# Kernel tuning notes

Measured on AMD Instinct MI355X. Metric: run time of the kernel, lower is better.

The kernel has to match this reference:

```python
import jax, jax.numpy as jnp
import numpy as np
import math

K, D_FEAT, L_FAC, N = 128, 1024, 16, 16384


def setup_inputs() -> dict:
    key = jax.random.key(0)
    k1, k2, k3, k4 = jax.random.split(key, 4)
    x = jax.random.normal(k1, (N, D_FEAT), dtype=jnp.float32)
    MU = 0.1 * jax.random.normal(k2, (K, D_FEAT), dtype=jnp.float32)
    A = 0.05 * jax.random.normal(k3, (K, D_FEAT, L_FAC), dtype=jnp.float32)
    # D must be positive (it is a per-feature noise std): uniform in [0.1, 0.5]
    D = jax.random.uniform(k4, (K, D_FEAT), dtype=jnp.float32, minval=0.1, maxval=0.5)
    PI = jnp.ones((K,), dtype=jnp.float32) / K
    return {"x": x, "PI": PI, "MU": MU, "A": A, "D": D}


def reference(x, PI, MU, A, D):
    # Faithful vectorized version of MFA._per_component_log_likelihood.
    k, d, l = A.shape
    iD = jnp.power(D, -2.0)                      # (K, d)  = 1/D^2
    iDA = iD[:, :, None] * A                     # (K, d, l)
    # Woodbury small matrix: L = I_l + A^T (iD * A)
    Lm = jnp.eye(l, dtype=A.dtype)[None] + jnp.einsum('kdl,kdm->klm', A, iDA)
    iL = jnp.linalg.inv(Lm)                      # (K, l, l)

    # y[k,n,:] = A^T (iD * (x_n - MU_k))  without materializing (K,N,d)
    y = jnp.einsum('nd,kdl->knl', x, iDA) - jnp.einsum('kd,kdl->kl', MU, iDA)[:, None, :]
    # term1[k,n] = sum_d iD[k,d] * (x_n - MU_k)^2, expanded to avoid (K,N,d)
    term1 = (jnp.einsum('nd,kd->kn', x * x, iD)
             - 2.0 * jnp.einsum('nd,kd->kn', x, iD * MU)
             + jnp.sum(iD * MU * MU, axis=1)[:, None])
    # quadratic correction: y^T iL y
    quad = jnp.einsum('knl,klm,knm->kn', y, iL, y)
    m_d = term1 - quad                           # (K, N) Mahalanobis distances

    det_L = jnp.linalg.slogdet(Lm)[1]            # (K,)
    log_det_Sigma = det_L - jnp.sum(jnp.log(iD), axis=1)
    log2pi = jnp.asarray(math.log(2.0 * math.pi), dtype=x.dtype)
    log_prob = -0.5 * ((d * log2pi + log_det_Sigma)[:, None] + m_d)  # (K, N)
    # NOTE: original adds raw PI (not log PI) -- replicated faithfully.
    return PI[None, :] + log_prob.T              # (N, K)
```

## Files before the change

### kernel.cpp

```cpp
#include <hip/hip_runtime.h>
#include <math.h>

typedef unsigned short ushort_t;
typedef unsigned char  uchar_t;
typedef __attribute__((ext_vector_type(8))) short short8v;
typedef __attribute__((ext_vector_type(4))) float f32x4;
typedef __attribute__((ext_vector_type(2))) long l64x2;

#define KCOMP 128
#define DF    1024
#define LF    16
#define NPTS  16384
#define LOG2PI 1.8378770664093453f

#define XQ_OFF    ((size_t)0)
#define XQ_BYTES  ((size_t)NPTS*DF)
#define BQ_OFF    (XQ_OFF + XQ_BYTES)
#define BQ_BYTES  ((size_t)2048*DF)
#define BSK_OFF   (BQ_OFF + BQ_BYTES)
#define BSK_BYTES ((size_t)KCOMP*2*DF*2)
#define CSK_OFF   (BSK_OFF + BSK_BYTES)
#define FULL_NEED (CSK_OFF + 512)

__device__ __forceinline__ ushort_t f2bf(float f) {
  union { float f; unsigned u; } v; v.f = f;
  unsigned u = v.u;
  return (ushort_t)((u + 0x7FFFu + ((u >> 16) & 1u)) >> 16);
}

#define GLOAD16(gp, lp) __builtin_amdgcn_global_load_lds( \
  (const __attribute__((address_space(1))) unsigned int*)(gp), \
  (__attribute__((address_space(3))) unsigned int*)(lp), 16, 0, 0)

#define DPPADD(x, ctrl) do { \
  int _yi = __builtin_amdgcn_update_dpp(0, __float_as_int(x), ctrl, 0xF, 0xF, true); \
  (x) += __int_as_float(_yi); } while (0)

__global__ __launch_bounds__(256) void mfa_pre(
    const float* __restrict__ PI, const float* __restrict__ MU,
    const float* __restrict__ A, const float* __restrict__ Dm,
    uchar_t* __restrict__ Bq, ushort_t* __restrict__ Bsk,
    float* __restrict__ csk)
{
  const int k = blockIdx.x, t = threadIdx.x;
  const int tl = t >> 4, tm = t & 15;
  __shared__ float As[64][16];
  __shared__ float iD64[64], MU64[64];
  __shared__ float R[16][17];
  __shared__ float rinv_s[16], zsh[16], bsh[16];
  __shared__ float red[64];
  __shared__ float sc_sumlog, sc_c3;

  float accL = 0.f, accb = 0.f, c3p = 0.f, slogp = 0.f;
  for (int ch = 0; ch < 16; ++ch) {
    __syncthreads();
    ((float4*)&As[0][0])[t] =
        ((const float4*)(A + (size_t)k*DF*LF + (size_t)ch*1024))[t];
    if (t < 64) {
      float dv = Dm[k*DF + ch*64 + t];
      iD64[t] = 1.f/(dv*dv);
      MU64[t] = MU[k*DF + ch*64 + t];
    }
    __syncthreads();
    #pragma unroll 4
    for (int dd = 0; dd < 64; ++dd)
      accL = fmaf(As[dd][tl]*iD64[dd], As[dd][tm], accL);
    if (tm == 0)
      for (int dd = 0; dd < 64; ++dd)
        accb = fmaf(iD64[dd]*MU64[dd], As[dd][tl], accb);
    if (t < 64) {
      c3p = fmaf(iD64[t]*MU64[t], MU64[t], c3p);
      slogp += logf(iD64[t]);
    }
  }
  __syncthreads();
  R[tl][tm] = accL + (tl == tm ? 1.f : 0.f);
  if (tm == 0) bsh[tl] = accb;
  if (t < 64) red[t] = slogp;
  __syncthreads();
  if (t == 0) { float s = 0.f; for (int i = 0; i < 64; ++i) s += red[i]; sc_sumlog = s; }
  __syncthreads();
  if (t < 64) red[t] = c3p;
  __syncthreads();
  if (t == 0) { float s = 0.f; for (int i = 0; i < 64; ++i) s += red[i]; sc_c3 = s; }

  for (int j = 0; j < 16; ++j) {
    __syncthreads();
    if (t == j) {
      float s = R[j][j];
      for (int i = 0; i < j; ++i) s -= R[j][i]*R[j][i];
      float rj = sqrtf(s);
      R[j][j] = rj; rinv_s[j] = 1.f/rj;
    }
    __syncthreads();
    if (t < 16 && t > j) {
      float s = R[t][j];
      for (int i = 0; i < j; ++i) s -= R[t][i]*R[j][i];
      R[t][j] = s * rinv_s[j];
    }
  }
  __syncthreads();
  if (t == 0) {
    float ldet = 0.f;
    for (int j = 0; j < 16; ++j) ldet += 2.f*logf(R[j][j]);
    float w[16], z[16];
    for (int j = 0; j < 16; ++j) {
      float s = bsh[j];
      for (int i = 0; i < j; ++i) s -= R[j][i]*w[i];
      w[j] = s*rinv_s[j];
    }
    for (int j = 15; j >= 0; --j) {
      float s = w[j];
      for (int i = j+1; i < 16; ++i) s -= R[i][j]*z[i];
      z[j] = s*rinv_s[j];
      zsh[j] = z[j];
    }
    float muh = sc_c3;
    for (int l = 0; l < 16; ++l) muh -= bsh[l]*zsh[l];
    csk[k] = PI[k] - 0.5f*((float)DF*LOG2PI + ldet - sc_sumlog) - 0.5f*muh;
  }
  __syncthreads();

  for (int it = 0; it < 4; ++it) {
    const int d = t + it*256;
    float dv = Dm[k*DF + d];
    float iD = 1.f/(dv*dv);
    float mu = MU[k*DF + d];
    float v[16], gg[16];
    #pragma unroll
    for (int l = 0; l < 16; ++l) v[l] = iD * A[((size_t)k*DF + d)*LF + l];
    #pragma unroll
    for (int j = 0; j < 16; ++j) {
      float s = v[j];
      #pragma unroll
      for (int i = 0; i < 16; ++i) if (i < j) s -= R[j][i]*gg[i];
      gg[j] = s * rinv_s[j];
    }
    float h = iD*mu;
    #pragma unroll
    for (int l = 0; l < 16; ++l) h -= v[l]*zsh[l];
    const int dd = d & 63;
    const size_t poff = (size_t)(d & ~63) + ((dd >> 3) & 3)*16 + (dd >> 5)*8 + (dd & 7);
    #pragma unroll
    for (int l = 0; l < 16; ++l) {
      int r8 = __builtin_amdgcn_cvt_pk_fp8_f32(gg[l], gg[l], 0, false);
      Bq[(size_t)(k*16 + l)*DF + poff] = (uchar_t)(r8 & 0xFF);
    }
    Bsk[(size_t)k*2*DF + d]      = f2bf(-2.f*h);
    Bsk[(size_t)k*2*DF + DF + d] = f2bf(iD);
  }
}

__global__ __launch_bounds__(256) void mfa_sk2q(
    const float* __restrict__ x, const ushort_t* __restrict__ Bsk,
    const float* __restrict__ csk, uchar_t* __restrict__ xq,
    float* __restrict__ out)
{
  __shared__ ushort_t xs[4096];
  __shared__ ushort_t x2s[4096];
  __shared__ ushort_t Bs[16384];
  const int t = threadIdx.x, lane = t & 63, wid = t >> 6;
  const int wc = wid;
  const int lr = lane & 15, lh = lane >> 4;
  const int n0 = blockIdx.x * 64;
  const int xr = t >> 2, xc = t & 3;

  f32x4 acc[4][2] = {};

  float4 v0, v1, v2, v3;
  {
    const float* xp = x + (size_t)(n0 + xr)*DF + xc*16;
    v0 = ((const float4*)xp)[0]; v1 = ((const float4*)xp)[1];
    v2 = ((const float4*)xp)[2]; v3 = ((const float4*)xp)[3];
  }

  for (int tt = 0; tt < 16; ++tt) {
    const int d0 = tt * 64;
    __syncthreads();
    {
      float e[16] = {v0.x,v0.y,v0.z,v0.w, v1.x,v1.y,v1.z,v1.w,
                     v2.x,v2.y,v2.z,v2.w, v3.x,v3.y,v3.z,v3.w};
      short8v b0, b1, q0, q1;
      #pragma unroll
      for (int i = 0; i < 8; ++i) {
        b0[i] = (short)f2bf(e[i]);     q0[i] = (short)f2bf(e[i]*e[i]);
        b1[i] = (short)f2bf(e[8+i]);   q1[i] = (short)f2bf(e[8+i]*e[8+i]);
      }
      const int ch0 = (xc*2) ^ (xr & 7), ch1 = (xc*2+1) ^ (xr & 7);
      *(short8v*)&xs[xr*64 + ch0*8]  = b0;
      *(short8v*)&xs[xr*64 + ch1*8]  = b1;
      *(short8v*)&x2s[xr*64 + ch0*8] = q0;
      *(short8v*)&x2s[xr*64 + ch1*8] = q1;
      int p0 = 0, p1 = 0, p2 = 0, p3 = 0;
      p0 = __builtin_amdgcn_cvt_pk_fp8_f32(e[0],  e[1],  p0, false);
      p0 = __builtin_amdgcn_cvt_pk_fp8_f32(e[2],  e[3],  p0, true);
      p1 = __builtin_amdgcn_cvt_pk_fp8_f32(e[4],  e[5],  p1, false);
      p1 = __builtin_amdgcn_cvt_pk_fp8_f32(e[6],  e[7],  p1, true);
      p2 = __builtin_amdgcn_cvt_pk_fp8_f32(e[8],  e[9],  p2, false);
      p2 = __builtin_amdgcn_cvt_pk_fp8_f32(e[10], e[11], p2, true);
      p3 = __builtin_amdgcn_cvt_pk_fp8_f32(e[12], e[13], p3, false);
      p3 = __builtin_amdgcn_cvt_pk_fp8_f32(e[14], e[15], p3, true);
      long lo = (long)(((unsigned long long)(unsigned)p1 << 32) | (unsigned)p0);
      long hi = (long)(((unsigned long long)(unsigned)p3 << 32) | (unsigned)p2);
      size_t base = (size_t)(n0 + xr)*DF + d0 + (xc & 1)*32 + (xc >> 1)*8;
      *(long*)&xq[base]      = lo;
      *(long*)&xq[base + 16] = hi;
    }
    #pragma unroll
    for (int j = 0; j < 8; ++j) {
      int v = (wid*8 + j)*8 + (lane >> 3);
      int g = (lane & 7) ^ (v & 7);
      const ushort_t* src = (v < 128)
        ? Bsk + (size_t)v*(2*DF) + d0 + g*8
        : Bsk + (size_t)(v - 128)*(2*DF) + DF + d0 + g*8;
      GLOAD16(src, (char*)Bs + (wid*8 + j)*1024);
    }
    __syncthreads();
    if (tt < 15) {
      const float* xp = x + (size_t)(n0 + xr)*DF + (d0 + 64) + xc*16;
      v0 = ((const float4*)xp)[0]; v1 = ((const float4*)xp)[1];
      v2 = ((const float4*)xp)[2]; v3 = ((const float4*)xp)[3];
    }
    __builtin_amdgcn_sched_barrier(0);
    #pragma unroll
    for (int ks = 0; ks < 2; ++ks) {
      const int cterm = ((ks*4 + lh) ^ (lr & 7)) * 8;
      short8v a_[4], a2_[4], bh[2], bi[2];
      #pragma unroll
      for (int rb = 0; rb < 4; ++rb) {
        a_[rb]  = *(const short8v*)&xs[(rb*16 + lr)*64 + cterm];
        a2_[rb] = *(const short8v*)&x2s[(rb*16 + lr)*64 + cterm];
      }
      #pragma unroll
      for (int cb = 0; cb < 2; ++cb) {
        int vh = wc*32 + cb*16 + lr;
        bh[cb] = *(const short8v*)&Bs[vh*64 + cterm];
        bi[cb] = *(const short8v*)&Bs[(128 + vh)*64 + cterm];
      }
      #pragma unroll
      for (int cb = 0; cb < 2; ++cb)
        #pragma unroll
        for (int rb = 0; rb < 4; ++rb) {
          acc[rb][cb] = __builtin_amdgcn_mfma_f32_16x16x32_bf16(a_[rb],  bh[cb], acc[rb][cb], 0,0,0);
          acc[rb][cb] = __builtin_amdgcn_mfma_f32_16x16x32_bf16(a2_[rb], bi[cb], acc[rb][cb], 0,0,0);
        }
    }
  }
  #pragma unroll
  for (int cb = 0; cb < 2; ++cb) {
    int comp = wc*32 + cb*16 + lr;
    float ck = csk[comp];
    #pragma unroll
    for (int rb = 0; rb < 4; ++rb)
      #pragma unroll
      for (int j = 0; j < 4; ++j) {
        int row = n0 + rb*16 + lh*4 + j;
        out[(size_t)row*KCOMP + comp] = ck - 0.5f*acc[rb][cb][j];
      }
  }
}

__global__ __launch_bounds__(512, 4) void mfa_gemm11(
    const uchar_t* __restrict__ xq, const uchar_t* __restrict__ Bq,
    float* __restrict__ out)
{
  __shared__ uchar_t smem[73728];
  const int t = threadIdx.x, lane = t & 63, wid = t >> 6;
  const int wm = wid & 1, wn = wid >> 1;
  const int lr = lane & 15, lh = lane >> 4;

  const int bid = blockIdx.x;
  const int xcd = bid & 7, ib = bid >> 3;
  const int rb = xcd*16 + (ib >> 3);
  const int cb = ib & 7;
  const int n0 = rb * 128, c0 = cb * 256;

  f32x4 acc[4][4] = {};

  const int js = (((lane & 3) ^ ((lane >> 3) & 3)) * 16);
  const uchar_t* srcP[3]; int dstO[3];
  #pragma unroll
  for (int q = 0; q < 3; ++q) {
    int id = wid*3 + q;
    if (id < 8) {
      int r = id*16 + (lane >> 2);
      srcP[q] = xq + (size_t)(n0 + r)*DF + js;
      dstO[q] = id*1024;
    } else {
      int cr = (id - 8)*16 + (lane >> 2);
      srcP[q] = Bq + (size_t)(c0 + cr)*DF + js;
      dstO[q] = 8192 + (id - 8)*1024;
    }
  }
  const int rsw = (lh ^ ((lr >> 1) & 3)) * 16;
  const int aO = (wm*64 + lr)*64 + rsw;
  const int bO = 8192 + (wn*64 + lr)*64 + rsw;

  #define STAGE11(slot, tt_) do { \
    _Pragma("unroll") \
    for (int q = 0; q < 3; ++q) \
      GLOAD16(srcP[q] + (tt_)*64, (char*)smem + (slot)*24576 + dstO[q] + ((lane)*16 & 1023)); \
  } while (0)

  STAGE11(0, 0);
  STAGE11(1, 1);

  for (int tt = 0; tt < 16; ++tt) {
    if (tt < 15) asm volatile("s_waitcnt vmcnt(3)" ::: "memory");
    else         asm volatile("s_waitcnt vmcnt(0)" ::: "memory");
    __builtin_amdgcn_s_barrier();
    if (tt + 2 <= 15) STAGE11((tt + 2) % 3, tt + 2);

    const char* lb = (const char*)smem + (tt % 3) * 24576;
    l64x2 a2[4], b2[4];
    #pragma unroll
    for (int rt = 0; rt < 4; ++rt) a2[rt] = *(const l64x2*)(lb + aO + rt*1024);
    #pragma unroll
    for (int ct = 0; ct < 4; ++ct) b2[ct] = *(const l64x2*)(lb + bO + ct*1024);

    __builtin_amdgcn_s_setprio(1);
    #pragma unroll
    for (int ct = 0; ct < 4; ++ct)
      #pragma unroll
      for (int rt = 0; rt < 4; ++rt)
        acc[rt][ct] = __builtin_amdgcn_mfma_f32_16x16x32_fp8_fp8(a2[rt][0], b2[ct][0], acc[rt][ct], 0,0,0);
    #pragma unroll
    for (int ct = 0; ct < 4; ++ct)
      #pragma unroll
      for (int rt = 0; rt < 4; ++rt)
        acc[rt][ct] = __builtin_amdgcn_mfma_f32_16x16x32_fp8_fp8(a2[rt][1], b2[ct][1], acc[rt][ct], 0,0,0);
    __builtin_amdgcn_s_setprio(0);
  }

  #pragma unroll
  for (int ct = 0; ct < 4; ++ct) {
    const int comp = cb*16 + wn*4 + ct;
    #pragma unroll
    for (int rt = 0; rt < 4; ++rt) {
      #pragma unroll
      for (int j = 0; j < 4; ++j) {
        float v = acc[rt][ct][j];
        float sq = v*v;
        DPPADD(sq, 0xB1);
        DPPADD(sq, 0x4E);
        DPPADD(sq, 0x124);
        DPPADD(sq, 0x128);
        if (lr == 0) {
          int row = n0 + wm*64 + rt*16 + lh*4 + j;
          size_t idx = (size_t)row * KCOMP + comp;
          out[idx] = out[idx] + 0.5f*sq;
        }
      }
    }
  }
}

#define FB_NG 8
#define FB_CG 288
#define FB_BN 128
#define FB_DT 32
#define FB_PITCH 40
#define FB_BMAT_ELEMS ((size_t)(FB_NG*FB_CG)*DF)
#define FB_CST_OFF (FB_BMAT_ELEMS*2)
#define FB_MUH_OFF (FB_CST_OFF + 512)

__global__ __launch_bounds__(256) void fb_pre(
    const float* __restrict__ PI, const float* __restrict__ MU,
    const float* __restrict__ A, const float* __restrict__ Dm,
    ushort_t* __restrict__ Bmat, float* __restrict__ cst, float* __restrict__ muh)
{
  const int k = blockIdx.x, t = threadIdx.x;
  const int tl = t >> 4, tm = t & 15;
  __shared__ float As[16][16], iDsh[16], MUsh[16];
  __shared__ float R[16][17], rinv[16], zsh[16], bsh[16];
  __shared__ float red[256];

  float accL = 0.f, accb = 0.f, slog = 0.f;
  for (int d0 = 0; d0 < DF; d0 += 16) {
    __syncthreads();
    As[tl][tm] = A[((size_t)k*DF + d0 + tl)*LF + tm];
    if (t < 16) {
      float dv = Dm[k*DF + d0 + t];
      iDsh[t] = 1.f/(dv*dv);
      MUsh[t] = MU[k*DF + d0 + t];
    }
    __syncthreads();
    #pragma unroll
    for (int dd = 0; dd < 16; ++dd)
      accL = fmaf(As[dd][tl]*iDsh[dd], As[dd][tm], accL);
    if (tm == 0) {
      #pragma unroll
      for (int dd = 0; dd < 16; ++dd)
        accb = fmaf(iDsh[dd]*MUsh[dd], As[dd][tl], accb);
    }
    if (t < 16) slog += logf(iDsh[t]);
  }
  __syncthreads();
  R[tl][tm] = accL + (tl == tm ? 1.f : 0.f);
  if (tm == 0) bsh[tl] = accb;
  red[t] = (t < 16) ? slog : 0.f;
  __syncthreads();
  float sumlogiD = 0.f;
  if (t == 0) { for (int i = 0; i < 16; ++i) sumlogiD += red[i]; }

  for (int j = 0; j < 16; ++j) {
    if (t == j) {
      float s = R[j][j];
      for (int i = 0; i < j; ++i) s -= R[j][i]*R[j][i];
      float rj = sqrtf(s);
      R[j][j] = rj; rinv[j] = 1.f/rj;
    }
    __syncthreads();
    if (t < 16 && t > j) {
      float s = R[t][j];
      for (int i = 0; i < j; ++i) s -= R[t][i]*R[j][i];
      R[t][j] = s * rinv[j];
    }
    __syncthreads();
  }

  float ldet = 0.f;
  if (t == 0) {
    #pragma unroll
    for (int j = 0; j < 16; ++j) ldet += 2.f*logf(R[j][j]);
    float w[16], z[16];
    #pragma unroll
    for (int j = 0; j < 16; ++j) {
      float s = bsh[j];
      #pragma unroll
      for (int i = 0; i < 16; ++i) if (i < j) s -= R[j][i]*w[i];
      w[j] = s*rinv[j];
    }
    #pragma unroll
    for (int j = 15; j >= 0; --j) {
      float s = w[j];
      #pragma unroll
      for (int i = 0; i < 16; ++i) if (i > j) s -= R[i][j]*z[i];
      z[j] = s*rinv[j];
      zsh[j] = z[j];
    }
  }
  __syncthreads();

  const int g = k >> 4, kl = k & 15;
  ushort_t* Bgp = Bmat + (size_t)g*FB_CG*DF;
  float muhp = 0.f;
  for (int itr = 0; itr < 4; ++itr) {
    int d = t + itr*256;
    float dv = Dm[k*DF + d];
    float iD = 1.f/(dv*dv);
    float mu = MU[k*DF + d];
    float v[16], gg[16];
    #pragma unroll
    for (int l = 0; l < 16; ++l) v[l] = iD * A[((size_t)k*DF + d)*LF + l];
    #pragma unroll
    for (int j = 0; j < 16; ++j) {
      float s = v[j];
      #pragma unroll
      for (int i = 0; i < 16; ++i) if (i < j) s -= R[j][i]*gg[i];
      gg[j] = s * rinv[j];
    }
    float h = iD*mu;
    #pragma unroll
    for (int l = 0; l < 16; ++l) h -= v[l]*zsh[l];
    muhp = fmaf(mu, h, muhp);
    #pragma unroll
    for (int l = 0; l < 16; ++l)
      Bgp[(size_t)(kl*16 + l)*DF + d] = f2bf(gg[l]);
    Bgp[(size_t)(256 + kl)*DF + d] = f2bf(h);
    Bgp[(size_t)(272 + kl)*DF + d] = f2bf(iD);
  }
  red[t] = muhp;
  __syncthreads();
  for (int s = 128; s > 0; s >>= 1) {
    if (t < s) red[t] += red[t + s];
    __syncthreads();
  }
  if (t == 0) {
    muh[k] = red[0];
    cst[k] = PI[k] - 0.5f*((float)DF*LOG2PI + ldet - sumlogiD);
  }
}

__global__ __launch_bounds__(512, 2) void fb_main(
    const float* __restrict__ x, const ushort_t* __restrict__ Bmat,
    const float* __restrict__ cst, const float* __restrict__ muh,
    float* __restrict__ out)
{
  __shared__ __align__(16) ushort_t smem[2*FB_BN*FB_PITCH + FB_CG*FB_PITCH];
  ushort_t* xs  = smem;
  ushort_t* x2s = smem + FB_BN*FB_PITCH;
  ushort_t* Bs  = smem + 2*FB_BN*FB_PITCH;

  const int t = threadIdx.x;
  const int lane = t & 63, wid = t >> 6;
  const int wr = wid & 3, wc = wid >> 2;
  const int lr = lane & 15, lh = lane >> 4;
  const int n0 = blockIdx.x * FB_BN;
  const int g  = blockIdx.y;

  f32x4 acc[2][9] = {};
  const int srow = t >> 2, sc = t & 3;

  int xoff[2];
  #pragma unroll
  for (int rt = 0; rt < 2; ++rt)
    xoff[rt] = (wr*32 + rt*16 + lr)*FB_PITCH + lh*8;
  int boff[9];
  #pragma unroll
  for (int ct = 0; ct < 9; ++ct)
    boff[ct] = (wc*144 + ct*16 + lr)*FB_PITCH + lh*8;

  for (int d0 = 0; d0 < DF; d0 += FB_DT) {
    __syncthreads();
    {
      const float* xp = x + (size_t)(n0 + srow)*DF + d0 + sc*8;
      float4 v0 = *(const float4*)xp;
      float4 v1 = *(const float4*)(xp + 4);
      float e[8] = {v0.x,v0.y,v0.z,v0.w,v1.x,v1.y,v1.z,v1.w};
      short8v xv, qv;
      #pragma unroll
      for (int i = 0; i < 8; ++i) {
        xv[i] = (short)f2bf(e[i]);
        qv[i] = (short)f2bf(e[i]*e[i]);
      }
      *(short8v*)&xs[srow*FB_PITCH + sc*8]  = xv;
      *(short8v*)&x2s[srow*FB_PITCH + sc*8] = qv;
    }
    for (int u = t; u < FB_CG*4; u += 512) {
      int col = u >> 2, c = u & 3;
      *(short8v*)&Bs[col*FB_PITCH + c*8] =
        *(const short8v*)&Bmat[((size_t)(g*FB_CG + col))*DF + d0 + c*8];
    }
    __syncthreads();

    short8v xf[2];
    #pragma unroll
    for (int rt = 0; rt < 2; ++rt) xf[rt] = *(short8v*)&xs[xoff[rt]];
    #pragma unroll
    for (int ct = 0; ct < 8; ++ct) {
      short8v bfr = *(short8v*)&Bs[boff[ct]];
      #pragma unroll
      for (int rt = 0; rt < 2; ++rt)
        acc[rt][ct] = __builtin_amdgcn_mfma_f32_16x16x32_bf16(xf[rt], bfr, acc[rt][ct], 0, 0, 0);
    }
    {
      short8v bfr = *(short8v*)&Bs[boff[8]];
      short8v a0 = xf[0], a1 = xf[1];
      if (wc) {
        a0 = *(short8v*)&x2s[xoff[0]];
        a1 = *(short8v*)&x2s[xoff[1]];
      }
      acc[0][8] = __builtin_amdgcn_mfma_f32_16x16x32_bf16(a0, bfr, acc[0][8], 0, 0, 0);
      acc[1][8] = __builtin_amdgcn_mfma_f32_16x16x32_bf16(a1, bfr, acc[1][8], 0, 0, 0);
    }
  }

  __syncthreads();
  float* s1v = (float*)smem;
  float* s2h = s1v + FB_BN*17;
  if (wc == 1) {
    #pragma unroll
    for (int rt = 0; rt < 2; ++rt)
      #pragma unroll
      for (int j = 0; j < 4; ++j) {
        int row = wr*32 + rt*16 + lh*4 + j;
        s2h[row*17 + lr] = acc[rt][7][j];
        s1v[row*17 + lr] = acc[rt][8][j];
      }
  }
  __syncthreads();

  const int nyt = wc ? 7 : 9;
  #pragma unroll
  for (int ct = 0; ct < 9; ++ct) {
    if (ct < nyt) {
      int comp = wc*9 + ct;
      int kk = g*16 + comp;
      float cstk = cst[kk], muhk = muh[kk];
      #pragma unroll
      for (int rt = 0; rt < 2; ++rt)
        #pragma unroll
        for (int j = 0; j < 4; ++j) {
          float yv = acc[rt][ct][j];
          float sq = yv*yv;
          sq += __shfl_xor(sq, 1);
          sq += __shfl_xor(sq, 2);
          sq += __shfl_xor(sq, 4);
          sq += __shfl_xor(sq, 8);
          int row = wr*32 + rt*16 + lh*4 + j;
          float s1 = s1v[row*17 + comp];
          float s2 = s2h[row*17 + comp];
          float res = cstk - 0.5f*(s1 - sq - 2.f*s2 + muhk);
          if (lr == 0) out[(size_t)(n0 + row)*KCOMP + kk] = res;
        }
    }
  }
}

extern "C" void kernel_launch(void* const* d_in, const int* in_sizes, int n_in,
                              void* d_out, int out_size, void* d_ws, size_t ws_size,
                              hipStream_t stream) {
  const float* x  = (const float*)d_in[0];
  const float* PI = (const float*)d_in[1];
  const float* MU = (const float*)d_in[2];
  const float* A  = (const float*)d_in[3];
  const float* Dm = (const float*)d_in[4];
  float* out = (float*)d_out;

  if (ws_size >= FULL_NEED) {
    uchar_t* xq   = (uchar_t*)((char*)d_ws + XQ_OFF);
    uchar_t* Bq   = (uchar_t*)((char*)d_ws + BQ_OFF);
    ushort_t* Bsk = (ushort_t*)((char*)d_ws + BSK_OFF);
    float* csk    = (float*)((char*)d_ws + CSK_OFF);

    mfa_pre<<<dim3(KCOMP), dim3(256), 0, stream>>>(PI, MU, A, Dm, Bq, Bsk, csk);
    mfa_sk2q<<<dim3(NPTS/64), dim3(256), 0, stream>>>(x, Bsk, csk, xq, out);
    mfa_gemm11<<<dim3((NPTS/128)*(2048/256)), dim3(512), 0, stream>>>(xq, Bq, out);
  } else {
    ushort_t* Bmat = (ushort_t*)d_ws;
    float* cstp = (float*)((char*)d_ws + FB_CST_OFF);
    float* muhp = (float*)((char*)d_ws + FB_MUH_OFF);
    fb_pre<<<dim3(KCOMP), dim3(256), 0, stream>>>(PI, MU, A, Dm, Bmat, cstp, muhp);
    fb_main<<<dim3(NPTS/FB_BN, FB_NG), dim3(512), 0, stream>>>(x, Bmat, cstp, muhp, out);
  }
}
```

Baseline: 151.7 us.

## Double threads per block in x-quantize/diagonal-term kernel, split rows across waves

The bf16 diagonal-term kernel moves from 256 to 512 threads per block. Each thread now converts 8 x-values instead of 16, and each wave computes half the rows for its 32 components. The fp8 store of x is deferred until after the barrier and an explicit waitcnt is added before it. This aims to raise memory-level parallelism and occupancy on a bandwidth-bound pass. The cost is more waves contending for the same LDS tile and an extra full wait each iteration.

```diff
diff --git a/kernel.cpp b/kernel.cpp
--- a/kernel.cpp
+++ b/kernel.cpp
@@ -151,7 +151,7 @@
   }
 }
 
-__global__ __launch_bounds__(256) void mfa_sk2q(
+__global__ __launch_bounds__(512) void mfa_sk5(
     const float* __restrict__ x, const ushort_t* __restrict__ Bsk,
     const float* __restrict__ csk, uchar_t* __restrict__ xq,
     float* __restrict__ out)
@@ -160,76 +160,71 @@
   __shared__ ushort_t x2s[4096];
   __shared__ ushort_t Bs[16384];
   const int t = threadIdx.x, lane = t & 63, wid = t >> 6;
-  const int wc = wid;
+  const int wc = wid & 3, rgrp = wid >> 2;
   const int lr = lane & 15, lh = lane >> 4;
   const int n0 = blockIdx.x * 64;
-  const int xr = t >> 2, xc = t & 3;
-
-  f32x4 acc[4][2] = {};
-
-  float4 v0, v1, v2, v3;
+  const int xr = t >> 3, c8 = t & 7;
+
+  f32x4 acc[2][2] = {};
+
+  float4 v0, v1;
   {
-    const float* xp = x + (size_t)(n0 + xr)*DF + xc*16;
+    const float* xp = x + (size_t)(n0 + xr)*DF + c8*8;
     v0 = ((const float4*)xp)[0]; v1 = ((const float4*)xp)[1];
-    v2 = ((const float4*)xp)[2]; v3 = ((const float4*)xp)[3];
   }
 
   for (int tt = 0; tt < 16; ++tt) {
     const int d0 = tt * 64;
     __syncthreads();
+    long xq_pack;
     {
-      float e[16] = {v0.x,v0.y,v0.z,v0.w, v1.x,v1.y,v1.z,v1.w,
-                     v2.x,v2.y,v2.z,v2.w, v3.x,v3.y,v3.z,v3.w};
-      short8v b0, b1, q0, q1;
+      float e[8] = {v0.x,v0.y,v0.z,v0.w, v1.x,v1.y,v1.z,v1.w};
+      short8v b, q;
       #pragma unroll
       for (int i = 0; i < 8; ++i) {
-        b0[i] = (short)f2bf(e[i]);     q0[i] = (short)f2bf(e[i]*e[i]);
-        b1[i] = (short)f2bf(e[8+i]);   q1[i] = (short)f2bf(e[8+i]*e[8+i]);
-      }
-      const int ch0 = (xc*2) ^ (xr & 7), ch1 = (xc*2+1) ^ (xr & 7);
-      *(short8v*)&xs[xr*64 + ch0*8]  = b0;
-      *(short8v*)&xs[xr*64 + ch1*8]  = b1;
-      *(short8v*)&x2s[xr*64 + ch0*8] = q0;
-      *(short8v*)&x2s[xr*64 + ch1*8] = q1;
-      int p0 = 0, p1 = 0, p2 = 0, p3 = 0;
-      p0 = __builtin_amdgcn_cvt_pk_fp8_f32(e[0],  e[1],  p0, false);
-      p0 = __builtin_amdgcn_cvt_pk_fp8_f32(e[2],  e[3],  p0, true);
-      p1 = __builtin_amdgcn_cvt_pk_fp8_f32(e[4],  e[5],  p1, false);
-      p1 = __builtin_amdgcn_cvt_pk_fp8_f32(e[6],  e[7],  p1, true);
-      p2 = __builtin_amdgcn_cvt_pk_fp8_f32(e[8],  e[9],  p2, false);
-      p2 = __builtin_amdgcn_cvt_pk_fp8_f32(e[10], e[11], p2, true);
-      p3 = __builtin_amdgcn_cvt_pk_fp8_f32(e[12], e[13], p3, false);
-      p3 = __builtin_amdgcn_cvt_pk_fp8_f32(e[14], e[15], p3, true);
-      long lo = (long)(((unsigned long long)(unsigned)p1 << 32) | (unsigned)p0);
-      long hi = (long)(((unsigned long long)(unsigned)p3 << 32) | (unsigned)p2);
-      size_t base = (size_t)(n0 + xr)*DF + d0 + (xc & 1)*32 + (xc >> 1)*8;
-      *(long*)&xq[base]      = lo;
-      *(long*)&xq[base + 16] = hi;
-    }
-    #pragma unroll
-    for (int j = 0; j < 8; ++j) {
-      int v = (wid*8 + j)*8 + (lane >> 3);
-      int g = (lane & 7) ^ (v & 7);
-      const ushort_t* src = (v < 128)
-        ? Bsk + (size_t)v*(2*DF) + d0 + g*8
-        : Bsk + (size_t)(v - 128)*(2*DF) + DF + d0 + g*8;
-      GLOAD16(src, (char*)Bs + (wid*8 + j)*1024);
-    }
-    __syncthreads();
+        b[i] = (short)f2bf(e[i]);
+        q[i] = (short)f2bf(e[i]*e[i]);
+      }
+      const int ch = c8 ^ (xr & 7);
+      *(short8v*)&xs[xr*64 + ch*8]  = b;
+      *(short8v*)&x2s[xr*64 + ch*8] = q;
+      int p0 = 0, p1 = 0;
+      p0 = __builtin_amdgcn_cvt_pk_fp8_f32(e[0], e[1], p0, false);
+      p0 = __builtin_amdgcn_cvt_pk_fp8_f32(e[2], e[3], p0, true);
+      p1 = __builtin_amdgcn_cvt_pk_fp8_f32(e[4], e[5], p1, false);
+      p1 = __builtin_amdgcn_cvt_pk_fp8_f32(e[6], e[7], p1, true);
+      xq_pack = (long)(((unsigned long long)(unsigned)p1 << 32) | (unsigned)p0);
+    }
+    #pragma unroll
+    for (int jj = 0; jj < 4; ++jj) {
+      int id = wid*4 + jj;
+      int vc = id*8 + (lane >> 3);
+      int g = (lane & 7) ^ (vc & 7);
+      const ushort_t* src = (vc < 128)
+        ? Bsk + (size_t)vc*(2*DF) + d0 + g*8
+        : Bsk + (size_t)(vc - 128)*(2*DF) + DF + d0 + g*8;
+      GLOAD16(src, (char*)Bs + id*1024);
+    }
+    asm volatile("s_waitcnt vmcnt(0) lgkmcnt(0)" ::: "memory");
+    __syncthreads();
+    {
+      const size_t perm = (size_t)(c8 & 3)*16 + (size_t)(c8 >> 2)*8;
+      *(long*)&xq[(size_t)(n0 + xr)*DF + d0 + perm] = xq_pack;
+    }
     if (tt < 15) {
-      const float* xp = x + (size_t)(n0 + xr)*DF + (d0 + 64) + xc*16;
+      const float* xp = x + (size_t)(n0 + xr)*DF + (d0 + 64) + c8*8;
       v0 = ((const float4*)xp)[0]; v1 = ((const float4*)xp)[1];
-      v2 = ((const float4*)xp)[2]; v3 = ((const float4*)xp)[3];
     }
     __builtin_amdgcn_sched_barrier(0);
     #pragma unroll
     for (int ks = 0; ks < 2; ++ks) {
       const int cterm = ((ks*4 + lh) ^ (lr & 7)) * 8;
-      short8v a_[4], a2_[4], bh[2], bi[2];
-      #pragma unroll
-      for (int rb = 0; rb < 4; ++rb) {
-        a_[rb]  = *(const short8v*)&xs[(rb*16 + lr)*64 + cterm];
-        a2_[rb] = *(const short8v*)&x2s[(rb*16 + lr)*64 + cterm];
+      short8v a_[2], a2_[2], bh[2], bi[2];
+      #pragma unroll
+      for (int rb = 0; rb < 2; ++rb) {
+        int row = rgrp*32 + rb*16 + lr;
+        a_[rb]  = *(const short8v*)&xs[row*64 + cterm];
+        a2_[rb] = *(const short8v*)&x2s[row*64 + cterm];
       }
       #pragma unroll
       for (int cb = 0; cb < 2; ++cb) {
@@ -240,7 +235,7 @@
       #pragma unroll
       for (int cb = 0; cb < 2; ++cb)
         #pragma unroll
-        for (int rb = 0; rb < 4; ++rb) {
+        for (int rb = 0; rb < 2; ++rb) {
           acc[rb][cb] = __builtin_amdgcn_mfma_f32_16x16x32_bf16(a_[rb],  bh[cb], acc[rb][cb], 0,0,0);
           acc[rb][cb] = __builtin_amdgcn_mfma_f32_16x16x32_bf16(a2_[rb], bi[cb], acc[rb][cb], 0,0,0);
         }
@@ -251,10 +246,10 @@
     int comp = wc*32 + cb*16 + lr;
     float ck = csk[comp];
     #pragma unroll
-    for (int rb = 0; rb < 4; ++rb)
+    for (int rb = 0; rb < 2; ++rb)
       #pragma unroll
       for (int j = 0; j < 4; ++j) {
-        int row = n0 + rb*16 + lh*4 + j;
+        int row = n0 + rgrp*32 + rb*16 + lh*4 + j;
         out[(size_t)row*KCOMP + comp] = ck - 0.5f*acc[rb][cb][j];
       }
   }
@@ -615,7 +610,7 @@
     float* csk    = (float*)((char*)d_ws + CSK_OFF);
 
     mfa_pre<<<dim3(KCOMP), dim3(256), 0, stream>>>(PI, MU, A, Dm, Bq, Bsk, csk);
-    mfa_sk2q<<<dim3(NPTS/64), dim3(256), 0, stream>>>(x, Bsk, csk, xq, out);
+    mfa_sk5<<<dim3(NPTS/64), dim3(512), 0, stream>>>(x, Bsk, csk, xq, out);
     mfa_gemm11<<<dim3((NPTS/128)*(2048/256)), dim3(512), 0, stream>>>(xq, Bq, out);
   } else {
     ushort_t* Bmat = (ushort_t*)d_ws;
```

After: 149.0 us. Within noise of the previous version (-1.7%).
